# Performance work log

Hardware: AMD Instinct MI355X
Metric: run time of the kernel (lower is better)

## Reference

```python
import jax, jax.numpy as jnp
import numpy as np

SCALES = (128.0, 256.0, 512.0)
ASPECT = (0.5, 1.0, 2.0)
K = 9
NMS_THR = 0.7
PRE_NMS_TOPK = 10000
POST_NMS_TOPK = 2000
MIN_SIZE = 16.0

def conv2d(x, w, b, pad):
    out = jax.lax.conv_general_dilated(x, w, (1, 1), [(pad, pad), (pad, pad)], dimension_numbers=('NCHW', 'OIHW', 'NCHW'))
    return out + b[None, :, None, None]

def generate_anchors(grid_h, grid_w, dtype):
    # Faithful to source: shifts are grid indices, NOT multiplied by stride (source bug kept).
    scales = jnp.asarray(SCALES, dtype)
    ar = jnp.asarray(ASPECT, dtype)
    h_ratio = jnp.sqrt(ar)
    w_ratio = 1.0 / h_ratio
    ws = (w_ratio[:, None] * scales[None, :]).reshape(-1)
    hs = (h_ratio[:, None] * scales[None, :]).reshape(-1)
    base = jnp.round(jnp.stack([-ws, -hs, ws, hs], axis=1) / 2.0)  # (9,4)
    sy, sx = jnp.meshgrid(jnp.arange(grid_h), jnp.arange(grid_w), indexing='ij')
    sx = sx.reshape(-1).astype(dtype)
    sy = sy.reshape(-1).astype(dtype)
    shifts = jnp.stack([sx, sy, sx, sy], axis=1)  # (H*W,4)
    return (shifts[:, None, :] + base[None, :, :]).reshape(-1, 4)  # (H*W*9,4)

def decode(box_pred, anchors):
    w = anchors[:, 2] - anchors[:, 0]
    h = anchors[:, 3] - anchors[:, 1]
    cx = anchors[:, 0] + 0.5 * w
    cy = anchors[:, 1] + 0.5 * h
    dx, dy, dw, dh = box_pred[:, 0], box_pred[:, 1], box_pred[:, 2], box_pred[:, 3]
    pcx = dx * w + cx
    pcy = dy * h + cy
    pw = jnp.exp(dw) * w
    ph = jnp.exp(dh) * h
    return jnp.stack([pcx - 0.5 * pw, pcy - 0.5 * ph, pcx + 0.5 * pw, pcy + 0.5 * ph], axis=1)

def nms_keep(boxes, valid, thr):
    # Greedy NMS on score-descending boxes; invalid (small) boxes never kept nor suppress others.
    n = boxes.shape[0]
    x1, y1, x2, y2 = boxes[:, 0], boxes[:, 1], boxes[:, 2], boxes[:, 3]
    areas = (x2 - x1) * (y2 - y1)
    idx = jnp.arange(n)
    def body(i, keep):
        xx1 = jnp.maximum(x1, x1[i]); yy1 = jnp.maximum(y1, y1[i])
        xx2 = jnp.minimum(x2, x2[i]); yy2 = jnp.minimum(y2, y2[i])
        inter = jnp.maximum(xx2 - xx1, 0.0) * jnp.maximum(yy2 - yy1, 0.0)
        iou = inter / (areas + areas[i] - inter)
        suppress = (iou > thr) & (idx > i) & keep[i]
        return keep & (~suppress)
    return jax.lax.fori_loop(0, n, body, valid)

def filter_proposals(proposals, cls_scores, img_h, img_w):
    scores = jax.nn.sigmoid(cls_scores.reshape(-1))
    top_scores, top_idx = jax.lax.top_k(scores, PRE_NMS_TOPK)  # sorted descending
    props = proposals[top_idx]
    x1 = jnp.clip(props[:, 0], 0.0, img_w); y1 = jnp.clip(props[:, 1], 0.0, img_h)
    x2 = jnp.clip(props[:, 2], 0.0, img_w); y2 = jnp.clip(props[:, 3], 0.0, img_h)
    props = jnp.stack([x1, y1, x2, y2], axis=1)
    valid = ((x2 - x1) >= MIN_SIZE) & ((y2 - y1) >= MIN_SIZE)
    keep = jax.lax.stop_gradient(nms_keep(jax.lax.stop_gradient(props), valid, NMS_THR))
    masked = jnp.where(keep, top_scores, -1.0)
    final_scores, final_idx = jax.lax.top_k(masked, POST_NMS_TOPK)  # order = score-descending (matches post-NMS sort)
    final_props = props[final_idx]
    valid_out = final_scores > 0.0  # sigmoid scores > 0, padding = -1
    return jnp.where(valid_out[:, None], final_props, 0.0), jnp.where(valid_out, final_scores, 0.0)

def setup_inputs():
    key = jax.random.key(0)
    ks = jax.random.split(key, 8)
    C = 512; GH = GW = 50
    feat = jax.random.normal(ks[0], (1, C, GH, GW), jnp.float32)
    image = jnp.zeros((1, 3, 800, 800), jnp.float32)
    gt_boxes = jax.random.uniform(ks[1], (8, 4), jnp.float32) * 800.0
    w_rpn = jax.random.normal(ks[2], (C, C, 3, 3), jnp.float32) * 0.01
    b_rpn = jnp.zeros((C,), jnp.float32)
    w_cls = jax.random.normal(ks[3], (K, C, 1, 1), jnp.float32) * 0.01
    b_cls = jnp.zeros((K,), jnp.float32)
    w_reg = jax.random.normal(ks[4], (4 * K, C, 1, 1), jnp.float32) * 0.01
    b_reg = jnp.zeros((4 * K,), jnp.float32)
    return {"image": image, "feat": feat, "gt_boxes": gt_boxes, "w_rpn": w_rpn, "b_rpn": b_rpn, "w_cls": w_cls, "b_cls": b_cls, "w_reg": w_reg, "b_reg": b_reg}

def reference(image, feat, gt_boxes, w_rpn, b_rpn, w_cls, b_cls, w_reg, b_reg):
    rpn_feat = jax.nn.relu(conv2d(feat, w_rpn, b_rpn, 1))
    cls = conv2d(rpn_feat, w_cls, b_cls, 0)      # (B,9,H,W)
    reg = conv2d(rpn_feat, w_reg, b_reg, 0)      # (B,36,H,W)
    B, _, gh, gw = feat.shape
    anchors = generate_anchors(gh, gw, feat.dtype)
    # flatten to anchor ordering (h, w, k) matching generate_anchors
    cls_flat = jnp.transpose(cls, (0, 2, 3, 1)).reshape(-1)
    reg_flat = jnp.transpose(reg.reshape(B, K, 4, gh, gw), (0, 3, 4, 1, 2)).reshape(-1, 4)
    proposals = decode(reg_flat, anchors)
    img_h, img_w = float(image.shape[-2]), float(image.shape[-1])
    return filter_proposals(proposals, cls_flat, img_h, img_w)
```

## Files before the change

### kernel.cpp

```cpp
#include <hip/hip_runtime.h>
#include <cmath>
#include <cstdint>
#include <cstddef>

typedef unsigned long long u64;
typedef unsigned int u32;

#define NPX   2500
#define NANCH 22500
#define PRE_TOPK 10000
#define NWORDS 160

struct AnchorBase { float b[36]; };

typedef __attribute__((ext_vector_type(8))) short bf16x8;
typedef __attribute__((ext_vector_type(4))) float f32x4;

__device__ inline unsigned short f2bf(float f) {
    u32 u = __float_as_uint(f);
    u32 r = u + 0x7fffu + ((u >> 16) & 1u);
    return (unsigned short)(r >> 16);
}
__device__ inline float bf2f(unsigned short h) {
    return __uint_as_float(((u32)h) << 16);
}

__global__ __launch_bounds__(256) void kprep(const float* __restrict__ feat,
                                             const float* __restrict__ wr,
                                             unsigned short* __restrict__ xthi,
                                             unsigned short* __restrict__ xtlo,
                                             unsigned short* __restrict__ whi,
                                             unsigned short* __restrict__ wlo)
{
    __shared__ float sh[4608];
    int bid = blockIdx.x;
    int t = threadIdx.x;
    if (bid < 416) {
        float (*tile)[65] = (float(*)[65])sh;
        int gr = bid >> 3;
        int cc = bid & 7;
        int tx = t & 63, ty = t >> 6;
        int y = gr - 1;
        bool rowok = (gr >= 1) && (gr <= 50);
#pragma unroll
        for (int i = 0; i < 16; ++i) {
            int c = i * 4 + ty;
            tile[c][tx] = (rowok && tx < 50)
                        ? feat[(size_t)(cc * 64 + c) * NPX + y * 50 + tx] : 0.f;
        }
        __syncthreads();
#pragma unroll
        for (int i = 0; i < 16; ++i) {
            int xp = i * 4 + ty;
            int cell = gr * 64 + xp;
            bool ok = rowok && xp >= 1 && xp <= 50;
            float v = ok ? tile[tx][xp - 1] : 0.f;
            unsigned short hi = f2bf(v);
            xthi[(size_t)cell * 512 + cc * 64 + tx] = hi;
            xtlo[(size_t)cell * 512 + cc * 64 + tx] = f2bf(v - bf2f(hi));
        }
    } else {
        int oc = bid - 416;
        for (int j = t; j < 4608; j += 256) sh[j] = wr[(size_t)oc * 4608 + j];
        __syncthreads();
        for (int k = t; k < 4608; k += 256) {
            int c = k & 511, tap = k >> 9;
            float v = sh[c * 9 + tap];
            unsigned short hi = f2bf(v);
            whi[(size_t)oc * 4608 + k] = hi;
            wlo[(size_t)oc * 4608 + k] = f2bf(v - bf2f(hi));
        }
    }
}

__global__ __launch_bounds__(256) void k1m(const unsigned short* __restrict__ xthi,
                                           const unsigned short* __restrict__ xtlo,
                                           const unsigned short* __restrict__ whi,
                                           const unsigned short* __restrict__ wlo,
                                           float* __restrict__ pk,
                                           int cptLog, int cptm1, int cptMul, int niter)
{
    __shared__ __align__(16) unsigned short Ah[8192];
    __shared__ __align__(16) unsigned short Al[8192];
    __shared__ __align__(16) unsigned short Bh[4096];
    __shared__ __align__(16) unsigned short Bl[4096];

    int t = threadIdx.x;
    int lane = t & 63, wave = t >> 6;
    int wo = wave & 1, wp = wave >> 1;
    int ocb = blockIdx.x, pxb = blockIdx.y, bs = blockIdx.z;
    int q = lane >> 4, m = lane & 15;
    int c0base = bs * cptMul;

    int g  = t & 7;
    int r0 = t >> 3;
    int ocA[4];
    int cellB[2];
#pragma unroll
    for (int i = 0; i < 4; ++i) ocA[i] = ocb * 128 + r0 + 32 * i;
#pragma unroll
    for (int i = 0; i < 2; ++i) {
        int opx = pxb * 64 + r0 + 32 * i;
        cellB[i] = (opx < NPX) ? ((opx / 50) + 1) * 64 + (opx % 50) + 1 : 190;
    }

    f32x4 acc[8];
    f32x4 zf = {0.f, 0.f, 0.f, 0.f};
#pragma unroll
    for (int i = 0; i < 8; ++i) acc[i] = zf;

    for (int it = 0; it < niter; ++it) {
        int tap = it >> cptLog;
        int cw  = it & cptm1;
        int c0  = c0base + cw * 64;
        int t3  = (tap * 43) >> 7;
        int tapoff = (t3 - 1) * 64 + (tap - t3 * 3) - 1;
#pragma unroll
        for (int i = 0; i < 4; ++i) {
            int rl = r0 + 32 * i;
            int la = rl * 64 + g * 8;
            size_t ga = (size_t)ocA[i] * 4608 + tap * 512 + c0 + g * 8;
            *(bf16x8*)(Ah + la) = *(const bf16x8*)(whi + ga);
            *(bf16x8*)(Al + la) = *(const bf16x8*)(wlo + ga);
        }
#pragma unroll
        for (int i = 0; i < 2; ++i) {
            int rl = r0 + 32 * i;
            int la = rl * 64 + g * 8;
            size_t gb = (size_t)(cellB[i] + tapoff) * 512 + c0 + g * 8;
            *(bf16x8*)(Bh + la) = *(const bf16x8*)(xthi + gb);
            *(bf16x8*)(Bl + la) = *(const bf16x8*)(xtlo + gb);
        }
        __syncthreads();
#pragma unroll
        for (int ks = 0; ks < 2; ++ks) {
            bf16x8 fah[4], fal[4], fbh[2], fbl[2];
#pragma unroll
            for (int mt = 0; mt < 4; ++mt) {
                int off = (wo * 64 + mt * 16 + m) * 64 + ks * 32 + q * 8;
                fah[mt] = *(const bf16x8*)(Ah + off);
                fal[mt] = *(const bf16x8*)(Al + off);
            }
#pragma unroll
            for (int nt = 0; nt < 2; ++nt) {
                int off = (wp * 32 + nt * 16 + m) * 64 + ks * 32 + q * 8;
                fbh[nt] = *(const bf16x8*)(Bh + off);
                fbl[nt] = *(const bf16x8*)(Bl + off);
            }
#pragma unroll
            for (int mt = 0; mt < 4; ++mt)
#pragma unroll
                for (int nt = 0; nt < 2; ++nt) {
                    f32x4 a = acc[mt * 2 + nt];
                    a = __builtin_amdgcn_mfma_f32_16x16x32_bf16(fal[mt], fbh[nt], a, 0, 0, 0);
                    a = __builtin_amdgcn_mfma_f32_16x16x32_bf16(fah[mt], fbl[nt], a, 0, 0, 0);
                    a = __builtin_amdgcn_mfma_f32_16x16x32_bf16(fah[mt], fbh[nt], a, 0, 0, 0);
                    acc[mt * 2 + nt] = a;
                }
        }
        __syncthreads();
    }
#pragma unroll
    for (int mt = 0; mt < 4; ++mt)
#pragma unroll
        for (int nt = 0; nt < 2; ++nt)
#pragma unroll
            for (int r = 0; r < 4; ++r) {
                int oc = ocb * 128 + wo * 64 + mt * 16 + q * 4 + r;
                int px = pxb * 64 + wp * 32 + nt * 16 + m;
                pk[((size_t)bs * 512 + oc) * 2560 + px] = acc[mt * 2 + nt][r];
            }
}

__global__ __launch_bounds__(256) void k2a_heads(const float* __restrict__ pk, int ns,
                                                 const float* __restrict__ br,
                                                 const float* __restrict__ wcls,
                                                 const float* __restrict__ wreg,
                                                 float* __restrict__ part)
{
    __shared__ float vt[64 * 64];
    __shared__ float Wl[45 * 64];
    int t  = threadIdx.x;
    int pb = blockIdx.x;
    int s  = blockIdx.y;
    int cb = s * 64;
    for (int e = t; e < 45 * 64; e += 256) {
        int u = e >> 6, c = e & 63;
        Wl[e] = (u < 9) ? wcls[u * 512 + cb + c] : wreg[(u - 9) * 512 + cb + c];
    }
    int pxl = t & 63, ug = t >> 6;
    int px = pb * 64 + pxl;
    bool ok = px < NPX;
#pragma unroll
    for (int i = 0; i < 16; ++i) {
        int c = ug * 16 + i;
        float v = 0.f;
        if (ok) {
            size_t bidx = (size_t)(cb + c) * 2560 + px;
            v = br[cb + c];
            for (int ks = 0; ks < ns; ++ks) v += pk[(size_t)ks * 512 * 2560 + bidx];
            v = v > 0.f ? v : 0.f;
        }
        vt[c * 64 + pxl] = v;
    }
    __syncthreads();
    int ubase = ug * 12;
    int ulim  = (45 - ubase < 12) ? (45 - ubase) : 12;
    float acc[12];
#pragma unroll
    for (int j = 0; j < 12; ++j) acc[j] = 0.f;
    for (int c = 0; c < 64; ++c) {
        float v = vt[c * 64 + pxl];
#pragma unroll
        for (int j = 0; j < 12; ++j)
            acc[j] = fmaf(v, Wl[(ubase + j) * 64 + c], acc[j]);
    }
    if (ok) {
        for (int j = 0; j < ulim; ++j)
            part[((size_t)s * 45 + ubase + j) * NPX + px] = acc[j];
    }
}

__global__ __launch_bounds__(256) void k2b_decode(const float* __restrict__ part,
                                                  const float* __restrict__ bcls,
                                                  const float* __restrict__ breg,
                                                  AnchorBase ab,
                                                  float* __restrict__ score,
                                                  float* __restrict__ bx1, float* __restrict__ by1,
                                                  float* __restrict__ bx2, float* __restrict__ by2,
                                                  u32* __restrict__ valid,
                                                  u64* __restrict__ key)
{
    int id = blockIdx.x * 256 + threadIdx.x;
    if (id >= NANCH) return;
    int k  = id / NPX;
    int px = id - k * NPX;

    float z  = bcls[k];
    float d0 = breg[k * 4 + 0], d1 = breg[k * 4 + 1];
    float d2 = breg[k * 4 + 2], d3 = breg[k * 4 + 3];
#pragma unroll
    for (int s = 0; s < 8; ++s) {
        const float* p = part + (size_t)s * 45 * NPX;
        z  += p[(size_t)k * NPX + px];
        d0 += p[(size_t)(9 + k * 4 + 0) * NPX + px];
        d1 += p[(size_t)(9 + k * 4 + 1) * NPX + px];
        d2 += p[(size_t)(9 + k * 4 + 2) * NPX + px];
        d3 += p[(size_t)(9 + k * 4 + 3) * NPX + px];
    }
    float sc = 1.f / (1.f + expf(-z));

    int yy = px / 50, xx = px - (px / 50) * 50;
    float fx = (float)xx, fy = (float)yy;
    float ax1 = fx + ab.b[k * 4 + 0], ay1 = fy + ab.b[k * 4 + 1];
    float ax2 = fx + ab.b[k * 4 + 2], ay2 = fy + ab.b[k * 4 + 3];
    float aw = ax2 - ax1, ah = ay2 - ay1;
    float cx = ax1 + 0.5f * aw, cy = ay1 + 0.5f * ah;
    float pcx = d0 * aw + cx, pcy = d1 * ah + cy;
    float pw = expf(d2) * aw, ph = expf(d3) * ah;
    float x1 = pcx - 0.5f * pw, y1 = pcy - 0.5f * ph;
    float x2 = pcx + 0.5f * pw, y2 = pcy + 0.5f * ph;
    x1 = fminf(fmaxf(x1, 0.f), 800.f);
    y1 = fminf(fmaxf(y1, 0.f), 800.f);
    x2 = fminf(fmaxf(x2, 0.f), 800.f);
    y2 = fminf(fmaxf(y2, 0.f), 800.f);
    u32 v = ((x2 - x1) >= 16.f) && ((y2 - y1) >= 16.f);

    int f = px * 9 + k;
    score[f] = sc;
    bx1[f] = x1; by1[f] = y1; bx2[f] = x2; by2[f] = y2;
    valid[f] = v;
    u32 sb = __float_as_uint(sc);
    key[f] = ((u64)(~sb) << 32) | (u32)f;
}

__global__ __launch_bounds__(256) void k3a_rank(const u64* __restrict__ key,
                                                u32* __restrict__ rankp)
{
    __shared__ __align__(16) u64 sk[2250];
    int t  = threadIdx.x;
    int jb = blockIdx.y;
    for (int e = t; e < 2250; e += 256) sk[e] = key[jb * 2250 + e];
    __syncthreads();
    int i0 = blockIdx.x * 1024 + t;
    int i1 = i0 + 256, i2 = i0 + 512, i3 = i0 + 768;
    u64 k0 = (i0 < NANCH) ? key[i0] : 0ull;
    u64 k1 = (i1 < NANCH) ? key[i1] : 0ull;
    u64 k2 = (i2 < NANCH) ? key[i2] : 0ull;
    u64 k3 = (i3 < NANCH) ? key[i3] : 0ull;
    u32 c0 = 0, c1 = 0, c2 = 0, c3 = 0;
    const ulonglong2* sk2 = (const ulonglong2*)sk;
#pragma unroll 5
    for (int j = 0; j < 1125; ++j) {
        ulonglong2 v = sk2[j];
        c0 += (v.x < k0) ? 1u : 0u;  c0 += (v.y < k0) ? 1u : 0u;
        c1 += (v.x < k1) ? 1u : 0u;  c1 += (v.y < k1) ? 1u : 0u;
        c2 += (v.x < k2) ? 1u : 0u;  c2 += (v.y < k2) ? 1u : 0u;
        c3 += (v.x < k3) ? 1u : 0u;  c3 += (v.y < k3) ? 1u : 0u;
    }
    size_t base = (size_t)jb * NANCH;
    if (i0 < NANCH) rankp[base + i0] = c0;
    if (i1 < NANCH) rankp[base + i1] = c1;
    if (i2 < NANCH) rankp[base + i2] = c2;
    if (i3 < NANCH) rankp[base + i3] = c3;
}

__global__ __launch_bounds__(256) void k3b_gather(const u32* __restrict__ rankp,
                                                  const float* __restrict__ score,
                                                  const float* __restrict__ bx1, const float* __restrict__ by1,
                                                  const float* __restrict__ bx2, const float* __restrict__ by2,
                                                  const u32* __restrict__ valid,
                                                  float* __restrict__ sS,
                                                  float* __restrict__ sx1, float* __restrict__ sy1,
                                                  float* __restrict__ sx2, float* __restrict__ sy2,
                                                  float4* __restrict__ sbox4,
                                                  u32* __restrict__ sInv)
{
    int i = blockIdx.x * 256 + threadIdx.x;
    if (i >= NANCH) return;
    u32 r = 0;
#pragma unroll
    for (int c = 0; c < 10; ++c) r += rankp[(size_t)c * NANCH + i];
    if (r >= PRE_TOPK) return;
    float x1 = bx1[i], y1 = by1[i], x2 = bx2[i], y2 = by2[i];
    sS[r] = score[i];
    sx1[r] = x1; sy1[r] = y1; sx2[r] = x2; sy2[r] = y2;
    float4 b4; b4.x = x1; b4.y = y1; b4.z = x2; b4.w = y2;
    sbox4[r] = b4;
    sInv[r] = valid[i] ? 0u : 1u;
}

__global__ __launch_bounds__(256) void k4_mat(const float4* __restrict__ sbox4,
                                              u64* __restrict__ rows,
                                              u64* __restrict__ selfw)
{
    int t = threadIdx.x, lane = t & 63, wave = t >> 6;
    int i = blockIdx.x * 4 + wave;
    if (i >= PRE_TOPK) return;
    float4 bi = sbox4[i];
    float ai = (bi.z - bi.x) * (bi.w - bi.y);
    int wd  = i >> 6;
    int ish = i & 63;
    u64 diagmask = ~((2ull << ish) - 1ull);
    u64* rowp = rows + (size_t)i * NWORDS;
    for (int w = wd; w < 157; ++w) {
        float4 bj = sbox4[(w << 6) + lane];
        float xx1 = fmaxf(bi.x, bj.x);
        float yy1 = fmaxf(bi.y, bj.y);
        float xx2 = fminf(bi.z, bj.z);
        float yy2 = fminf(bi.w, bj.w);
        float iw = fmaxf(xx2 - xx1, 0.f);
        float ih = fmaxf(yy2 - yy1, 0.f);
        float inter = iw * ih;
        float aj = (bj.z - bj.x) * (bj.w - bj.y);
        float uni = ai + aj - inter;
        u64 b = __ballot(inter > 0.7f * uni);
        if (w == wd)  b &= diagmask;
        if (w == 156) b &= 0xFFFFull;
        if (lane == 0) {
            rowp[w] = b;
            if (w == wd) selfw[i] = b;
        }
    }
}

__global__ __launch_bounds__(64) void k5_scan(const u64* __restrict__ rows,
                                              const u64* __restrict__ selfw,
                                              const u32* __restrict__ sInv,
                                              const float* __restrict__ sS,
                                              const float* __restrict__ sx1, const float* __restrict__ sy1,
                                              const float* __restrict__ sx2, const float* __restrict__ sy2,
                                              float* __restrict__ out)
{
    __shared__ int keptList[2000];
    __shared__ int kcnt;
    int l = threadIdx.x;
    auto bw = [&](int w) -> u64 {
        const uint4* p = (const uint4*)(sInv + (size_t)w * 64);
        u64 v = 0;
#pragma unroll
        for (int j = 0; j < 16; ++j) {
            uint4 q = p[j];
            v |= ((u64)(q.x != 0) << (j * 4))     | ((u64)(q.y != 0) << (j * 4 + 1))
               | ((u64)(q.z != 0) << (j * 4 + 2)) | ((u64)(q.w != 0) << (j * 4 + 3));
        }
        return v;
    };
    auto rdlane64 = [&](u64 v, int src) -> u64 {
        u32 lo = __builtin_amdgcn_readlane((u32)v, src);
        u32 hi = __builtin_amdgcn_readlane((u32)(v >> 32), src);
        return ((u64)hi << 32) | lo;
    };
    u64 r0 = bw(l);
    u64 r1 = bw(64 + l);
    u64 r2 = (l < 32) ? bw(128 + l) : ~0ull;

    u64 s0 = selfw[(size_t)0 * 64 + l];
    u64 s1 = selfw[(size_t)1 * 64 + l];
    u64 s2 = selfw[(size_t)2 * 64 + l];
    u64 s3 = selfw[(size_t)3 * 64 + l];
    u64 s4 = selfw[(size_t)4 * 64 + l];
    u64 s5 = selfw[(size_t)5 * 64 + l];
    u64 s6 = selfw[(size_t)6 * 64 + l];
    u64 s7 = selfw[(size_t)7 * 64 + l];

    int cnt = 0;
    bool done = false;
    for (int w = 0; w < 157; ++w) {
        u64 swreg = s0;
        s0 = s1; s1 = s2; s2 = s3; s3 = s4; s4 = s5; s5 = s6; s6 = s7;
        s7 = (w + 8 < 157) ? selfw[(size_t)(w + 8) * 64 + l] : 0ull;

        int slot = w >> 6, owner = w & 63;
        u64 val = (slot == 0) ? r0 : (slot == 1) ? r1 : r2;
        u64 rw = rdlane64(val, owner);
        u64 wmask = (w == 156) ? 0xFFFFull : ~0ull;
        u64 av = (~rw) & wmask;

        u64 km = 0;
        while (av) {
            int b = __builtin_ctzll(av);
            u64 sw = rdlane64(swreg, b);
            km |= 1ull << b;
            av &= ~(1ull << b);
            av &= ~sw;
        }
        u64 kk = km;
        while (kk) {
            int bsx[16];
            int nb = 0;
            while (kk && nb < 16) {
                int b = __builtin_ctzll(kk);
                kk &= kk - 1;
                bsx[nb++] = b;
            }
            u64 a0 = 0, a1 = 0, a2 = 0;
#pragma unroll
            for (int u = 0; u < 16; ++u) {
                if (u < nb) {
                    int i = (w << 6) + bsx[u];
                    if (l == 0 && cnt + u < 2000) keptList[cnt + u] = i;
                    const u64* rp = rows + (size_t)i * NWORDS;
                    a0 |= rp[l];
                    a1 |= rp[64 + l];
                    if (l < 32) a2 |= rp[128 + l];
                }
            }
            r0 |= a0; r1 |= a1; r2 |= a2;
            cnt += nb;
            if (cnt >= 2000) { done = true; break; }
        }
        if (done) break;
    }
    if (l == 0) kcnt = (cnt < 2000) ? cnt : 2000;
    __syncthreads();
    int K = kcnt;
    for (int r = l; r < 2000; r += 64) {
        if (r < K) {
            int j = keptList[r];
            out[r * 4 + 0] = sx1[j];
            out[r * 4 + 1] = sy1[j];
            out[r * 4 + 2] = sx2[j];
            out[r * 4 + 3] = sy2[j];
            out[8000 + r]  = sS[j];
        } else {
            out[r * 4 + 0] = 0.f; out[r * 4 + 1] = 0.f;
            out[r * 4 + 2] = 0.f; out[r * 4 + 3] = 0.f;
            out[8000 + r]  = 0.f;
        }
    }
}

extern "C" void kernel_launch(void* const* d_in, const int* in_sizes, int n_in,
                              void* d_out, int out_size, void* d_ws, size_t ws_size,
                              hipStream_t stream)
{
    (void)in_sizes; (void)n_in; (void)out_size;
    const float* feat = (const float*)d_in[1];
    const float* wrpn = (const float*)d_in[3];
    const float* brpn = (const float*)d_in[4];
    const float* wcls = (const float*)d_in[5];
    const float* bcls = (const float*)d_in[6];
    const float* wreg = (const float*)d_in[7];
    const float* breg = (const float*)d_in[8];
    float* out = (float*)d_out;

    int ns = (ws_size >= 58195968) ? 8 : (ws_size >= 37224448) ? 4 : 2;
    int cpt     = 8 / ns;
    int cptLog  = (ns == 2) ? 2 : (ns == 4) ? 1 : 0;
    int cptm1   = cpt - 1;
    int cptMul  = cpt * 64;
    int niter   = 9 * cpt;
    size_t pkB = (size_t)ns * 512 * 2560 * 4;

    char* ws = (char*)d_ws;
    float* pk = (float*)ws;
    unsigned short* Xthi = (unsigned short*)(ws + pkB);
    unsigned short* Xtlo = Xthi + (size_t)52 * 64 * 512;
    unsigned short* Whi  = (unsigned short*)(ws + pkB + 6815744);
    unsigned short* Wlo  = Whi + (size_t)512 * 4608;

    char* sm = ws + pkB;
    float* score = (float*)(sm + 0);
    float* bx1   = (float*)(sm + 90000);
    float* by1   = (float*)(sm + 180000);
    float* bx2   = (float*)(sm + 270000);
    float* by2   = (float*)(sm + 360000);
    u32*   valid = (u32*)  (sm + 450000);
    u64*   key   = (u64*)  (sm + 540000);
    u32*   rankp = (u32*)  (sm + 720000);
    float* sS    = (float*)(sm + 1620000);
    float* sx1   = (float*)(sm + 1660000);
    float* sy1   = (float*)(sm + 1700000);
    float* sx2   = (float*)(sm + 1740000);
    float* sy2   = (float*)(sm + 1780000);
    u32*   sInv  = (u32*)  (sm + 1820000);
    u64*   selfw = (u64*)  (sm + 1860960);
    float4* sbox4= (float4*)(sm + 1942880);
    float* part  = (float*)(sm + 2106720);
    u64*   rows  = (u64*)  (sm + 2106720);

    AnchorBase ab;
    {
        const float scales[3] = {128.f, 256.f, 512.f};
        const float aspect[3] = {0.5f, 1.f, 2.f};
        for (int ai = 0; ai < 3; ++ai) {
            float hr = sqrtf(aspect[ai]);
            float wratio = 1.0f / hr;
            for (int si = 0; si < 3; ++si) {
                float wsz = wratio * scales[si];
                float hsz = hr * scales[si];
                int a = ai * 3 + si;
                ab.b[a * 4 + 0] = rintf(-wsz / 2.0f);
                ab.b[a * 4 + 1] = rintf(-hsz / 2.0f);
                ab.b[a * 4 + 2] = rintf( wsz / 2.0f);
                ab.b[a * 4 + 3] = rintf( hsz / 2.0f);
            }
        }
    }

    kprep    <<<928, 256, 0, stream>>>(feat, wrpn, Xthi, Xtlo, Whi, Wlo);
    k1m      <<<dim3(4, 40, ns), 256, 0, stream>>>(Xthi, Xtlo, Whi, Wlo, pk,
                                                   cptLog, cptm1, cptMul, niter);
    k2a_heads<<<dim3(40, 8), 256, 0, stream>>>(pk, ns, brpn, wcls, wreg, part);
    k2b_decode<<<88, 256, 0, stream>>>(part, bcls, breg, ab, score, bx1, by1, bx2, by2, valid, key);
    k3a_rank <<<dim3(22, 10), 256, 0, stream>>>(key, rankp);
    k3b_gather<<<88, 256, 0, stream>>>(rankp, score, bx1, by1, bx2, by2, valid,
                                       sS, sx1, sy1, sx2, sy2, sbox4, sInv);
    hipMemsetAsync(rows, 0, (size_t)PRE_TOPK * NWORDS * 8, stream);
    k4_mat   <<<2500, 256, 0, stream>>>(sbox4, rows, selfw);
    k5_scan  <<<1, 64, 0, stream>>>(rows, selfw, sInv, sS, sx1, sy1, sx2, sy2, out);
}
```

Baseline: 368.2 us.

## Process NMS scan in groups of four words with cross-word self masks

k4_mat now writes a transposed 4x4 block of intra-group suppression words (selfgT) per 256-box group instead of only the diagonal word. The single-wave scan resolves four 64-bit words at a time: each kept bit immediately clears suppressed bits in the later words of the group via readlane, and row ORs are batched up to 32 kept boxes. Row words that are already finished are skipped. This shortens the serial chain of global row reads per word, at the cost of more registers (32 prefetched u64 masks) and extra writes in k4_mat.

```diff
diff --git a/kernel.cpp b/kernel.cpp
--- a/kernel.cpp
+++ b/kernel.cpp
@@ -332,7 +332,7 @@
 
 __global__ __launch_bounds__(256) void k4_mat(const float4* __restrict__ sbox4,
                                               u64* __restrict__ rows,
-                                              u64* __restrict__ selfw)
+                                              u64* __restrict__ selfgT)
 {
     int t = threadIdx.x, lane = t & 63, wave = t >> 6;
     int i = blockIdx.x * 4 + wave;
@@ -340,9 +340,16 @@
     float4 bi = sbox4[i];
     float ai = (bi.z - bi.x) * (bi.w - bi.y);
     int wd  = i >> 6;
+    int gb  = wd & ~3;
+    int g   = wd >> 2;
+    int kk  = wd & 3;
     int ish = i & 63;
     u64 diagmask = ~((2ull << ish) - 1ull);
     u64* rowp = rows + (size_t)i * NWORDS;
+    if (lane == 0) {
+        for (int w0 = gb; w0 < wd; ++w0)
+            selfgT[(size_t)g * 1024 + (w0 - gb) * 256 + kk * 64 + ish] = 0ull;
+    }
     for (int w = wd; w < 157; ++w) {
         float4 bj = sbox4[(w << 6) + lane];
         float xx1 = fmaxf(bi.x, bj.x);
@@ -359,13 +366,14 @@
         if (w == 156) b &= 0xFFFFull;
         if (lane == 0) {
             rowp[w] = b;
-            if (w == wd) selfw[i] = b;
-        }
-    }
-}
-
-__global__ __launch_bounds__(64) void k5_scan(const u64* __restrict__ rows,
-                                              const u64* __restrict__ selfw,
+            if (w < gb + 4)
+                selfgT[(size_t)g * 1024 + (w - gb) * 256 + kk * 64 + ish] = b;
+        }
+    }
+}
+
+__global__ __launch_bounds__(64, 1) void k5_scan(const u64* __restrict__ rows,
+                                              const u64* __restrict__ selfgT,
                                               const u32* __restrict__ sInv,
                                               const float* __restrict__ sS,
                                               const float* __restrict__ sx1, const float* __restrict__ sy1,
@@ -386,71 +394,123 @@
         }
         return v;
     };
-    auto rdlane64 = [&](u64 v, int src) -> u64 {
+    auto rdl = [&](u64 v, int src) -> u64 {
         u32 lo = __builtin_amdgcn_readlane((u32)v, src);
         u32 hi = __builtin_amdgcn_readlane((u32)(v >> 32), src);
         return ((u64)hi << 32) | lo;
     };
+    auto ldsg = [&](int g, int m, int k) -> u64 {
+        return selfgT[(size_t)g * 1024 + m * 256 + k * 64 + l];
+    };
     u64 r0 = bw(l);
     u64 r1 = bw(64 + l);
     u64 r2 = (l < 32) ? bw(128 + l) : ~0ull;
 
-    u64 s0 = selfw[(size_t)0 * 64 + l];
-    u64 s1 = selfw[(size_t)1 * 64 + l];
-    u64 s2 = selfw[(size_t)2 * 64 + l];
-    u64 s3 = selfw[(size_t)3 * 64 + l];
-    u64 s4 = selfw[(size_t)4 * 64 + l];
-    u64 s5 = selfw[(size_t)5 * 64 + l];
-    u64 s6 = selfw[(size_t)6 * 64 + l];
-    u64 s7 = selfw[(size_t)7 * 64 + l];
+    auto avInit = [&](int w) -> u64 {
+        if (w > 156) return 0ull;
+        int slot = w >> 6, owner = w & 63;
+        u64 val = (slot == 0) ? r0 : (slot == 1) ? r1 : r2;
+        u64 rw = rdl(val, owner);
+        u64 wmask = (w == 156) ? 0xFFFFull : ~0ull;
+        return (~rw) & wmask;
+    };
+
+    u64 c00 = ldsg(0,0,0), c01 = ldsg(0,0,1), c02 = ldsg(0,0,2), c03 = ldsg(0,0,3);
+    u64 c10 = ldsg(0,1,0), c11 = ldsg(0,1,1), c12 = ldsg(0,1,2), c13 = ldsg(0,1,3);
+    u64 c20 = ldsg(0,2,0), c21 = ldsg(0,2,1), c22 = ldsg(0,2,2), c23 = ldsg(0,2,3);
+    u64 c30 = ldsg(0,3,0), c31 = ldsg(0,3,1), c32 = ldsg(0,3,2), c33 = ldsg(0,3,3);
+    u64 n00 = ldsg(1,0,0), n01 = ldsg(1,0,1), n02 = ldsg(1,0,2), n03 = ldsg(1,0,3);
+    u64 n10 = ldsg(1,1,0), n11 = ldsg(1,1,1), n12 = ldsg(1,1,2), n13 = ldsg(1,1,3);
+    u64 n20 = ldsg(1,2,0), n21 = ldsg(1,2,1), n22 = ldsg(1,2,2), n23 = ldsg(1,2,3);
+    u64 n30 = ldsg(1,3,0), n31 = ldsg(1,3,1), n32 = ldsg(1,3,2), n33 = ldsg(1,3,3);
 
     int cnt = 0;
     bool done = false;
-    for (int w = 0; w < 157; ++w) {
-        u64 swreg = s0;
-        s0 = s1; s1 = s2; s2 = s3; s3 = s4; s4 = s5; s5 = s6; s6 = s7;
-        s7 = (w + 8 < 157) ? selfw[(size_t)(w + 8) * 64 + l] : 0ull;
-
-        int slot = w >> 6, owner = w & 63;
-        u64 val = (slot == 0) ? r0 : (slot == 1) ? r1 : r2;
-        u64 rw = rdlane64(val, owner);
-        u64 wmask = (w == 156) ? 0xFFFFull : ~0ull;
-        u64 av = (~rw) & wmask;
-
-        u64 km = 0;
-        while (av) {
-            int b = __builtin_ctzll(av);
-            u64 sw = rdlane64(swreg, b);
-            km |= 1ull << b;
-            av &= ~(1ull << b);
-            av &= ~sw;
-        }
-        u64 kk = km;
-        while (kk) {
-            int bsx[16];
-            int nb = 0;
-            while (kk && nb < 16) {
-                int b = __builtin_ctzll(kk);
-                kk &= kk - 1;
-                bsx[nb++] = b;
-            }
+    for (int g = 0; g < 40 && !done; ++g) {
+        int wb = g << 2;
+        u64 av0 = avInit(wb + 0);
+        u64 av1 = avInit(wb + 1);
+        u64 av2 = avInit(wb + 2);
+        u64 av3 = avInit(wb + 3);
+        u64 km0 = 0, km1 = 0, km2 = 0, km3 = 0;
+        while (av0) {
+            int b = __builtin_ctzll((unsigned long long)av0);
+            u64 s0 = rdl(c00, b), s1 = rdl(c10, b), s2 = rdl(c20, b), s3 = rdl(c30, b);
+            km0 |= 1ull << b;
+            av0 = (av0 & (av0 - 1)) & ~s0;
+            av1 &= ~s1; av2 &= ~s2; av3 &= ~s3;
+        }
+        while (av1) {
+            int b = __builtin_ctzll((unsigned long long)av1);
+            u64 s1 = rdl(c11, b), s2 = rdl(c21, b), s3 = rdl(c31, b);
+            km1 |= 1ull << b;
+            av1 = (av1 & (av1 - 1)) & ~s1;
+            av2 &= ~s2; av3 &= ~s3;
+        }
+        while (av2) {
+            int b = __builtin_ctzll((unsigned long long)av2);
+            u64 s2 = rdl(c22, b), s3 = rdl(c32, b);
+            km2 |= 1ull << b;
+            av2 = (av2 & (av2 - 1)) & ~s2;
+            av3 &= ~s3;
+        }
+        while (av3) {
+            int b = __builtin_ctzll((unsigned long long)av3);
+            u64 s3 = rdl(c33, b);
+            km3 |= 1ull << b;
+            av3 = (av3 & (av3 - 1)) & ~s3;
+        }
+        bool need0 = (wb + 4) < 64;
+        bool need1 = (wb + 4) < 128;
+        int bsx[32];
+        int nb = 0;
+        auto flush = [&]() {
+            if (nb == 0) return;
             u64 a0 = 0, a1 = 0, a2 = 0;
 #pragma unroll
-            for (int u = 0; u < 16; ++u) {
+            for (int u = 0; u < 32; ++u) {
                 if (u < nb) {
-                    int i = (w << 6) + bsx[u];
-                    if (l == 0 && cnt + u < 2000) keptList[cnt + u] = i;
-                    const u64* rp = rows + (size_t)i * NWORDS;
-                    a0 |= rp[l];
-                    a1 |= rp[64 + l];
+                    const u64* rp = rows + (size_t)bsx[u] * NWORDS;
+                    if (need0) a0 |= rp[l];
+                    if (need1) a1 |= rp[64 + l];
                     if (l < 32) a2 |= rp[128 + l];
                 }
             }
-            r0 |= a0; r1 |= a1; r2 |= a2;
-            cnt += nb;
-            if (cnt >= 2000) { done = true; break; }
-        }
-        if (done) break;
+            if (need0) r0 |= a0;
+            if (need1) r1 |= a1;
+            r2 |= a2;
+            nb = 0;
+        };
+#pragma unroll
+        for (int kk = 0; kk < 4; ++kk) {
+            u64 mask = (kk == 0) ? km0 : (kk == 1) ? km1 : (kk == 2) ? km2 : km3;
+            int wbase = (wb + kk) << 6;
+            while (mask) {
+                int b = __builtin_ctzll((unsigned long long)mask);
+                mask &= mask - 1;
+                int idx = wbase + b;
+                if (l == 0 && cnt < 2000) keptList[cnt] = idx;
+                ++cnt;
+                bsx[nb++] = idx;
+                if (nb == 32) flush();
+                if (cnt >= 2000) { done = true; break; }
+            }
+            if (done) break;
+        }
+        if (!done) {
+            flush();
+            c00 = n00; c01 = n01; c02 = n02; c03 = n03;
+            c10 = n10; c11 = n11; c12 = n12; c13 = n13;
+            c20 = n20; c21 = n21; c22 = n22; c23 = n23;
+            c30 = n30; c31 = n31; c32 = n32; c33 = n33;
+            int gn = g + 2;
+            if (gn < 40) {
+                n00 = ldsg(gn,0,0); n01 = ldsg(gn,0,1); n02 = ldsg(gn,0,2); n03 = ldsg(gn,0,3);
+                n10 = ldsg(gn,1,0); n11 = ldsg(gn,1,1); n12 = ldsg(gn,1,2); n13 = ldsg(gn,1,3);
+                n20 = ldsg(gn,2,0); n21 = ldsg(gn,2,1); n22 = ldsg(gn,2,2); n23 = ldsg(gn,2,3);
+                n30 = ldsg(gn,3,0); n31 = ldsg(gn,3,1); n32 = ldsg(gn,3,2); n33 = ldsg(gn,3,3);
+            }
+        }
     }
     if (l == 0) kcnt = (cnt < 2000) ? cnt : 2000;
     __syncthreads();
@@ -515,10 +575,10 @@
     float* sx2   = (float*)(sm + 1740000);
     float* sy2   = (float*)(sm + 1780000);
     u32*   sInv  = (u32*)  (sm + 1820000);
-    u64*   selfw = (u64*)  (sm + 1860960);
     float4* sbox4= (float4*)(sm + 1942880);
     float* part  = (float*)(sm + 2106720);
     u64*   rows  = (u64*)  (sm + 2106720);
+    u64*   selfgT= (u64*)  (sm + 14906720);
 
     AnchorBase ab;
     {
@@ -548,6 +608,6 @@
     k3b_gather<<<88, 256, 0, stream>>>(rankp, score, bx1, by1, bx2, by2, valid,
                                        sS, sx1, sy1, sx2, sy2, sbox4, sInv);
     hipMemsetAsync(rows, 0, (size_t)PRE_TOPK * NWORDS * 8, stream);
-    k4_mat   <<<2500, 256, 0, stream>>>(sbox4, rows, selfw);
-    k5_scan  <<<1, 64, 0, stream>>>(rows, selfw, sInv, sS, sx1, sy1, sx2, sy2, out);
-}
+    k4_mat   <<<2500, 256, 0, stream>>>(sbox4, rows, selfgT);
+    k5_scan  <<<1, 64, 0, stream>>>(rows, selfgT, sInv, sS, sx1, sy1, sx2, sy2, out);
+}
```

Result: slower. 389.0 us (+5.6%).
